# Performance work log

Hardware: AMD Instinct MI355X
Metric: run time of the kernel (lower is better)

The kernel has to match this reference:

```python
import jax, jax.numpy as jnp
import numpy as np

H = 512          # hidden_size
E = 2 * H        # bidirectional embed dim
NH = 8           # attention heads
HD = E // NH     # head dim = 128
SEQ = 10         # hard-coded seq_len in forward
IN = 512         # input_size
OUT = 256        # output_size


def _gru_dir(gi, Whh, bhh, reverse):
    # gi: [B,S,3H] precomputed input-side gate pre-activations
    if reverse:
        gi = gi[:, ::-1]
    B = gi.shape[0]
    h0 = jnp.zeros((B, H), gi.dtype)

    def step(h, gi_t):
        gh = h @ Whh.T + bhh                      # [B,3H]
        ir, iz, inn = jnp.split(gi_t, 3, axis=-1)
        hr, hz, hn = jnp.split(gh, 3, axis=-1)
        r = jax.nn.sigmoid(ir + hr)
        z = jax.nn.sigmoid(iz + hz)
        n = jnp.tanh(inn + r * hn)
        h_new = (1.0 - z) * n + z * h
        return h_new, h_new

    _, hs = jax.lax.scan(step, h0, jnp.swapaxes(gi, 0, 1))
    hs = jnp.swapaxes(hs, 0, 1)                   # [B,S,H]
    if reverse:
        hs = hs[:, ::-1]
    return hs


def _bi_gru_layer(x_seq, Wih, Whh, bih, bhh):
    # Wih: [2, 3H, in]; dir 0 = forward, dir 1 = backward
    outs = []
    for d, rev in ((0, False), (1, True)):
        gi = jnp.einsum('bsi,gi->bsg', x_seq, Wih[d]) + bih[d]
        outs.append(_gru_dir(gi, Whh[d], bhh[d], rev))
    return jnp.concatenate(outs, axis=-1)         # [B,S,2H]


def _attention(x, in_proj_w, in_proj_b, out_proj_w, out_proj_b):
    B, S, _ = x.shape
    qkv = x @ in_proj_w.T + in_proj_b             # [B,S,3E]
    q, k, v = jnp.split(qkv, 3, axis=-1)
    q = q.reshape(B, S, NH, HD)
    k = k.reshape(B, S, NH, HD)
    v = v.reshape(B, S, NH, HD)
    scores = jnp.einsum('bqhd,bkhd->bhqk', q, k) / jnp.sqrt(jnp.asarray(HD, x.dtype))
    attn = jax.nn.softmax(scores, axis=-1)
    o = jnp.einsum('bhqk,bkhd->bqhd', attn, v).reshape(B, S, E)
    return o @ out_proj_w.T + out_proj_b


def _forward(x, Wp, bp, Wih0, Whh0, bih0, bhh0, Wih1, Whh1, bih1, bhh1,
             in_proj_w, in_proj_b, out_proj_w, out_proj_b, W1, b1, W2, b2):
    x_proj = x @ Wp.T + bp                        # [B,H]
    phases = 2.0 * np.pi * np.arange(SEQ) / SEQ
    cos = jnp.asarray(np.cos(phases), x.dtype)    # [S]
    sin = jnp.asarray(np.sin(phases), x.dtype)
    rolled = jnp.roll(x_proj, shift=1, axis=-1)
    x_seq = (x_proj[:, None, :] * (1.0 + 0.1 * cos[None, :, None])
             + 0.05 * sin[None, :, None] * rolled[:, None, :])  # [B,S,H]
    h1 = _bi_gru_layer(x_seq, Wih0, Whh0, bih0, bhh0)           # [B,S,2H]
    gru_out = _bi_gru_layer(h1, Wih1, Whh1, bih1, bhh1)         # [B,S,2H]
    attn_out = _attention(gru_out, in_proj_w, in_proj_b, out_proj_w, out_proj_b)
    aggregated = jnp.mean(gru_out + attn_out, axis=1)           # [B,2H]
    hid = jnp.tanh(aggregated @ W1.T + b1)                      # [B,128]
    return hid @ W2.T + b2                                      # [B,OUT]


def setup_inputs() -> dict:
    key = jax.random.key(0)
    ks = jax.random.split(key, 24)
    s = 1.0 / np.sqrt(H)
    u = lambda k, shape: jax.random.uniform(k, shape, jnp.float32, -s, s)
    return {
        'x': jax.random.normal(ks[0], (4096, IN), jnp.float32),
        'Wp': u(ks[1], (H, IN)), 'bp': u(ks[2], (H,)),
        'Wih0': u(ks[3], (2, 3 * H, H)), 'Whh0': u(ks[4], (2, 3 * H, H)),
        'bih0': u(ks[5], (2, 3 * H)), 'bhh0': u(ks[6], (2, 3 * H)),
        'Wih1': u(ks[7], (2, 3 * H, 2 * H)), 'Whh1': u(ks[8], (2, 3 * H, H)),
        'bih1': u(ks[9], (2, 3 * H)), 'bhh1': u(ks[10], (2, 3 * H)),
        'in_proj_w': u(ks[11], (3 * E, E)), 'in_proj_b': u(ks[12], (3 * E,)),
        'out_proj_w': u(ks[13], (E, E)), 'out_proj_b': u(ks[14], (E,)),
        'W1': u(ks[15], (128, E)), 'b1': u(ks[16], (128,)),
        'W2': u(ks[17], (OUT, 128)), 'b2': u(ks[18], (OUT,)),
    }


def reference(x, Wp, bp, Wih0, Whh0, bih0, bhh0, Wih1, Whh1, bih1, bhh1,
              in_proj_w, in_proj_b, out_proj_w, out_proj_b, W1, b1, W2, b2):
    return _forward(x, Wp, bp, Wih0, Whh0, bih0, bhh0, Wih1, Whh1, bih1, bhh1,
                    in_proj_w, in_proj_b, out_proj_w, out_proj_b, W1, b1, W2, b2)
```

## Files before the change

### kernel.cpp

```cpp
#include <hip/hip_runtime.h>
#include <math.h>


#define SEQ 10

typedef unsigned short bf16u;
typedef __attribute__((ext_vector_type(8))) short short8v;
typedef __attribute__((ext_vector_type(4))) float f32x4;

#define AS1 __attribute__((address_space(1)))
#define AS3 __attribute__((address_space(3)))

__device__ __forceinline__ float b2f(bf16u u) {
    union { unsigned int i; float f; } v; v.i = ((unsigned int)u) << 16; return v.f;
}
__device__ __forceinline__ bf16u f2b(float f) {
    union { float f; unsigned int i; } v; v.f = f;
    unsigned int r = (v.i + 0x7FFFu + ((v.i >> 16) & 1u)) >> 16;
    return (bf16u)r;
}
__device__ __forceinline__ float fast_sigm(float x) { return 1.0f / (1.0f + __expf(-x)); }
__device__ __forceinline__ float fast_tanh(float x) {
    float e = __expf(-2.0f * x);
    return 2.0f / (1.0f + e) - 1.0f;
}

__global__ void cvt_f2b(const float* __restrict__ src, bf16u* __restrict__ dst, int n4)
{
    int i = blockIdx.x * 256 + threadIdx.x;
    if (i < n4) {
        float4 v = ((const float4*)src)[i];
        ushort4 u; u.x = f2b(v.x); u.y = f2b(v.y); u.z = f2b(v.z); u.w = f2b(v.w);
        ((ushort4*)dst)[i] = u;
    }
}

template <typename TC>
__global__ __launch_bounds__(512) void gemm_mfma256(
    const bf16u* __restrict__ A, long long sAz, int lda,
    const bf16u* __restrict__ W, long long sWz,
    const float* __restrict__ bias, long long sBz,
    TC* __restrict__ C, long long sCz, int ldc,
    int K, int act)
{
    __shared__ bf16u As[2][256 * 64];
    __shared__ bf16u Ws[2][256 * 64];

    const int z = blockIdx.z;
    A += (long long)z * sAz;
    W += (long long)z * sWz;
    C += (long long)z * sCz;
    const float* bz = bias ? (bias + (long long)z * sBz) : nullptr;

    const int gx = gridDim.x;
    const int nwg = gx * gridDim.y;
    const int orig = blockIdx.y * gx + blockIdx.x;
    const int q = nwg >> 3, rres = nwg & 7;
    const int xcd = orig & 7, loc = orig >> 3;
    const int wgid = (xcd < rres ? xcd * (q + 1) : rres * (q + 1) + (xcd - rres) * q) + loc;
    const int bm = (wgid / gx) * 256;
    const int bn = (wgid % gx) * 256;

    const int tid = threadIdx.x;
    const int lane = tid & 63;
    const int w = tid >> 6;
    const int wm = w >> 2;
    const int wn = w & 3;
    const int l15 = lane & 15;
    const int lk8 = (lane >> 4) * 8;
    const int swz = (l15 & 7) << 3;

    f32x4 acc[8][4];
#pragma unroll
    for (int i = 0; i < 8; ++i)
#pragma unroll
        for (int j = 0; j < 4; ++j)
#pragma unroll
            for (int r = 0; r < 4; ++r) acc[i][j][r] = 0.0f;

    const int srow = lane >> 3;
    const int scol = ((lane & 7) ^ srow) * 8;
    const bf16u* Ag[4];
    const bf16u* Wg[4];
    int loff[4];
#pragma unroll
    for (int p = 0; p < 4; ++p) {
        const int r = p * 64 + w * 8 + srow;
        Ag[p] = A + (long long)(bm + r) * lda + scol;
        Wg[p] = W + (long long)(bn + r) * K + scol;
        loff[p] = (p * 8 + w) * 512;
    }

    auto stage = [&](int kt, int b) {
        const long long k1 = (long long)kt << 6;
#pragma unroll
        for (int p = 0; p < 4; ++p) {
            __builtin_amdgcn_global_load_lds((const AS1 void*)(Ag[p] + k1),
                (AS3 void*)(&As[b][loff[p]]), 16, 0, 0);
            __builtin_amdgcn_global_load_lds((const AS1 void*)(Wg[p] + k1),
                (AS3 void*)(&Ws[b][loff[p]]), 16, 0, 0);
        }
    };
    auto compute = [&](int b) {
#pragma unroll
        for (int ks = 0; ks < 2; ++ks) {
            const int ko = (ks * 32 + lk8) ^ swz;
            short8v af[8], bfr[4];
#pragma unroll
            for (int i = 0; i < 8; ++i)
                af[i] = *(const short8v*)(&As[b][(wm * 128 + i * 16 + l15) * 64 + ko]);
#pragma unroll
            for (int i = 0; i < 4; ++i)
                bfr[i] = *(const short8v*)(&Ws[b][(wn * 64 + i * 16 + l15) * 64 + ko]);
#pragma unroll
            for (int mi = 0; mi < 8; ++mi)
#pragma unroll
                for (int ni = 0; ni < 4; ++ni)
                    acc[mi][ni] = __builtin_amdgcn_mfma_f32_16x16x32_bf16(
                        af[mi], bfr[ni], acc[mi][ni], 0, 0, 0);
        }
    };

    const int nt = K >> 6;

    stage(0, 0);
    stage(1, 1);

    for (int t = 0; t < nt - 1; ++t) {
        asm volatile("s_waitcnt vmcnt(8)" ::: "memory");
        __builtin_amdgcn_s_barrier();
        asm volatile("" ::: "memory");
        compute(t & 1);
        asm volatile("" ::: "memory");
        __builtin_amdgcn_s_barrier();
        if (t + 2 < nt) stage(t + 2, t & 1);
    }
    asm volatile("s_waitcnt vmcnt(0)" ::: "memory");
    __builtin_amdgcn_s_barrier();
    compute((nt - 1) & 1);

    const int r0 = (lane >> 4) * 4;
#pragma unroll
    for (int mi = 0; mi < 8; ++mi) {
#pragma unroll
        for (int ni = 0; ni < 4; ++ni) {
            const int col = bn + wn * 64 + ni * 16 + l15;
            float badd = bz ? bz[col] : 0.0f;
#pragma unroll
            for (int r = 0; r < 4; ++r) {
                const long long row = bm + wm * 128 + mi * 16 + r0 + r;
                float v = acc[mi][ni][r] + badd;
                if (act) v = tanhf(v);
                if constexpr (sizeof(TC) == 4) ((float*)C)[row * ldc + col] = v;
                else                           ((bf16u*)C)[row * ldc + col] = f2b(v);
            }
        }
    }
}

template <typename TC>
__global__ __launch_bounds__(256) void gemm_mfma128p(
    const bf16u* __restrict__ A, long long sAz, int lda,
    const bf16u* __restrict__ W, long long sWz,
    const float* __restrict__ bias, long long sBz,
    TC* __restrict__ C, long long sCz, int ldc,
    int K, int act)
{
    __shared__ bf16u As[2][128 * 64];
    __shared__ bf16u Ws[2][128 * 64];

    const int z = blockIdx.z;
    A += (long long)z * sAz;
    W += (long long)z * sWz;
    C += (long long)z * sCz;
    const float* bz = bias ? (bias + (long long)z * sBz) : nullptr;

    const int gx = gridDim.x;
    const int nwg = gx * gridDim.y;
    const int orig = blockIdx.y * gx + blockIdx.x;
    const int q = nwg >> 3, rres = nwg & 7;
    const int xcd = orig & 7, loc = orig >> 3;
    const int wgid = (xcd < rres ? xcd * (q + 1) : rres * (q + 1) + (xcd - rres) * q) + loc;
    const int bm = (wgid / gx) * 128;
    const int bn = (wgid % gx) * 128;

    const int tid = threadIdx.x;
    const int lane = tid & 63;
    const int w = tid >> 6;
    const int wm = w >> 1;
    const int wn = w & 1;
    const int l15 = lane & 15;
    const int lk8 = (lane >> 4) * 8;
    const int swz = (l15 & 7) << 3;

    f32x4 acc[4][4];
#pragma unroll
    for (int i = 0; i < 4; ++i)
#pragma unroll
        for (int j = 0; j < 4; ++j)
#pragma unroll
            for (int r = 0; r < 4; ++r) acc[i][j][r] = 0.0f;

    const int srow = lane >> 3;
    const int scol = ((lane & 7) ^ srow) * 8;
    const bf16u* Ag[4];
    const bf16u* Wg[4];
    int loff[4];
#pragma unroll
    for (int p = 0; p < 4; ++p) {
        const int r = p * 32 + w * 8 + srow;
        Ag[p] = A + (long long)(bm + r) * lda + scol;
        Wg[p] = W + (long long)(bn + r) * K + scol;
        loff[p] = (p * 32 + w * 8) * 64;
    }

    auto stage = [&](int kt, int b) {
        const long long k1 = (long long)kt << 6;
#pragma unroll
        for (int p = 0; p < 4; ++p) {
            __builtin_amdgcn_global_load_lds((const AS1 void*)(Ag[p] + k1),
                (AS3 void*)(&As[b][loff[p]]), 16, 0, 0);
            __builtin_amdgcn_global_load_lds((const AS1 void*)(Wg[p] + k1),
                (AS3 void*)(&Ws[b][loff[p]]), 16, 0, 0);
        }
    };
    auto compute = [&](int b) {
#pragma unroll
        for (int ks = 0; ks < 2; ++ks) {
            const int ko = (ks * 32 + lk8) ^ swz;
            short8v af[4], bfr[4];
#pragma unroll
            for (int i = 0; i < 4; ++i)
                af[i] = *(const short8v*)(&As[b][(wm * 64 + i * 16 + l15) * 64 + ko]);
#pragma unroll
            for (int i = 0; i < 4; ++i)
                bfr[i] = *(const short8v*)(&Ws[b][(wn * 64 + i * 16 + l15) * 64 + ko]);
            __builtin_amdgcn_s_setprio(1);
#pragma unroll
            for (int mi = 0; mi < 4; ++mi)
#pragma unroll
                for (int ni = 0; ni < 4; ++ni)
                    acc[mi][ni] = __builtin_amdgcn_mfma_f32_16x16x32_bf16(
                        af[mi], bfr[ni], acc[mi][ni], 0, 0, 0);
            __builtin_amdgcn_s_setprio(0);
        }
    };

    const int nt = K >> 6;

    stage(0, 0);
    stage(1, 1);

    for (int t = 0; t < nt - 1; ++t) {
        asm volatile("s_waitcnt vmcnt(8)" ::: "memory");
        __builtin_amdgcn_s_barrier();
        asm volatile("" ::: "memory");
        compute(t & 1);
        asm volatile("" ::: "memory");
        __builtin_amdgcn_s_barrier();
        if (t + 2 < nt) stage(t + 2, t & 1);
    }
    asm volatile("s_waitcnt vmcnt(0)" ::: "memory");
    __builtin_amdgcn_s_barrier();
    compute((nt - 1) & 1);

    const int r0 = (lane >> 4) * 4;
#pragma unroll
    for (int mi = 0; mi < 4; ++mi) {
#pragma unroll
        for (int ni = 0; ni < 4; ++ni) {
            const int col = bn + wn * 64 + ni * 16 + l15;
            float badd = bz ? bz[col] : 0.0f;
#pragma unroll
            for (int r = 0; r < 4; ++r) {
                const long long row = bm + wm * 64 + mi * 16 + r0 + r;
                float v = acc[mi][ni][r] + badd;
                if (act) v = tanhf(v);
                if constexpr (sizeof(TC) == 4) ((float*)C)[row * ldc + col] = v;
                else                           ((bf16u*)C)[row * ldc + col] = f2b(v);
            }
        }
    }
}

template <typename TC>
__global__ __launch_bounds__(256) void gemm_mfma(
    const bf16u* __restrict__ A, long long sAz, int lda,
    const bf16u* __restrict__ W, long long sWz,
    const float* __restrict__ bias, long long sBz,
    TC* __restrict__ C, long long sCz, int ldc,
    int K, int act)
{
    __shared__ bf16u As[128 * 64];
    __shared__ bf16u Ws[128 * 64];

    const int z = blockIdx.z;
    A += (long long)z * sAz;
    W += (long long)z * sWz;
    C += (long long)z * sCz;
    const float* bz = bias ? (bias + (long long)z * sBz) : nullptr;

    const int gx = gridDim.x;
    const int nwg = gx * gridDim.y;
    const int orig = blockIdx.y * gx + blockIdx.x;
    const int q = nwg >> 3, rres = nwg & 7;
    const int xcd = orig & 7, loc = orig >> 3;
    const int wgid = (xcd < rres ? xcd * (q + 1) : rres * (q + 1) + (xcd - rres) * q) + loc;
    const int bm = (wgid / gx) * 128;
    const int bn = (wgid % gx) * 128;

    const int tid = threadIdx.x;
    const int lane = tid & 63;
    const int wave = tid >> 6;
    const int wr = (wave >> 1) * 64;
    const int wc = (wave & 1) * 64;
    const int l15 = lane & 15;
    const int lk8 = (lane >> 4) * 8;

    f32x4 acc[4][4];
#pragma unroll
    for (int i = 0; i < 4; ++i)
#pragma unroll
        for (int j = 0; j < 4; ++j)
#pragma unroll
            for (int r = 0; r < 4; ++r) acc[i][j][r] = 0.0f;

    const int sr = wave * 32 + (lane >> 3);
    const int sc = (lane & 7) * 8;
    const bf16u* Ag = A + (long long)(bm + sr) * lda + sc;
    const bf16u* Wg = W + (long long)(bn + sr) * K + sc;
    bf16u* Al = As + wave * 32 * 64;
    bf16u* Wl = Ws + wave * 32 * 64;

    for (int k0 = 0; k0 < K; k0 += 64) {
#pragma unroll
        for (int p = 0; p < 4; ++p) {
            __builtin_amdgcn_global_load_lds(
                (const AS1 void*)(Ag + k0 + (long long)(8 * p) * lda),
                (AS3 void*)(Al + 8 * p * 64), 16, 0, 0);
            __builtin_amdgcn_global_load_lds(
                (const AS1 void*)(Wg + k0 + (long long)(8 * p) * K),
                (AS3 void*)(Wl + 8 * p * 64), 16, 0, 0);
        }
        __syncthreads();
#pragma unroll
        for (int ks = 0; ks < 2; ++ks) {
            short8v af[4], bfr[4];
#pragma unroll
            for (int i = 0; i < 4; ++i)
                af[i] = *(const short8v*)(As + (wr + i * 16 + l15) * 64 + ks * 32 + lk8);
#pragma unroll
            for (int i = 0; i < 4; ++i)
                bfr[i] = *(const short8v*)(Ws + (wc + i * 16 + l15) * 64 + ks * 32 + lk8);
#pragma unroll
            for (int mi = 0; mi < 4; ++mi)
#pragma unroll
                for (int ni = 0; ni < 4; ++ni)
                    acc[mi][ni] = __builtin_amdgcn_mfma_f32_16x16x32_bf16(
                        af[mi], bfr[ni], acc[mi][ni], 0, 0, 0);
        }
        __syncthreads();
    }

    const int r0 = (lane >> 4) * 4;
#pragma unroll
    for (int mi = 0; mi < 4; ++mi) {
#pragma unroll
        for (int ni = 0; ni < 4; ++ni) {
            const int col = bn + wc + ni * 16 + l15;
            float badd = bz ? bz[col] : 0.0f;
#pragma unroll
            for (int r = 0; r < 4; ++r) {
                const long long row = bm + wr + mi * 16 + r0 + r;
                float v = acc[mi][ni][r] + badd;
                if (act) v = tanhf(v);
                if constexpr (sizeof(TC) == 4) ((float*)C)[row * ldc + col] = v;
                else                           ((bf16u*)C)[row * ldc + col] = f2b(v);
            }
        }
    }
}

template <int LAYER, bool FIRST>
__global__ __launch_bounds__(256) void gru_step(
    const bf16u* __restrict__ Hb,
    const bf16u* __restrict__ Whh,
    const float* __restrict__ bhh,
    const bf16u* __restrict__ P0,
    const bf16u* __restrict__ P1,
    const float* __restrict__ bih,
    const bf16u* __restrict__ GIT,
    const float* __restrict__ hprev,
    float* __restrict__ hnext,
    bf16u* __restrict__ hnextb,
    bf16u* __restrict__ hout,
    int t, int CB)
{
    __shared__ bf16u As[2][64 * 64];
    __shared__ bf16u Ws[2][96 * 64];

    const int z = blockIdx.z;
    const int bn = blockIdx.x * 32;
    const int bm = blockIdx.y * 64;
    const int tid = threadIdx.x;
    const int lane = tid & 63;
    const int wave = tid >> 6;
    const int wm = wave >> 1;
    const int wn = wave & 1;
    const int l15 = lane & 15;
    const int lk8 = (lane >> 4) * 8;
    const int swz = (l15 & 7) << 3;

    f32x4 acc[3][2];
#pragma unroll
    for (int g = 0; g < 3; ++g)
#pragma unroll
        for (int i = 0; i < 2; ++i)
#pragma unroll
            for (int r = 0; r < 4; ++r) acc[g][i][r] = 0.0f;

    if constexpr (!FIRST) {
        const bf16u* hsrc = Hb + (long long)z * CB * 512;
        const bf16u* wsrc = Whh + (long long)z * 1536 * 512;

        const int srow = lane >> 3;
        const int sc = ((lane & 7) ^ srow) * 8;
        const bf16u* Ag = hsrc + (long long)(bm + 16 * wave + srow) * 512 + sc;
        const bf16u* Wg[3];
#pragma unroll
        for (int p = 0; p < 3; ++p) {
            const int lr = 24 * wave + 8 * p + srow;
            const int g = lr >> 5, c = lr & 31;
            Wg[p] = wsrc + (long long)(g * 512 + bn + c) * 512 + sc;
        }

        auto stage = [&](int kt, int b) {
            const long long k0 = (long long)kt << 6;
#pragma unroll
            for (int p = 0; p < 2; ++p)
                __builtin_amdgcn_global_load_lds(
                    (const AS1 void*)(Ag + k0 + (long long)(8 * p) * 512),
                    (AS3 void*)(&As[b][(16 * wave + 8 * p) * 64]), 16, 0, 0);
#pragma unroll
            for (int p = 0; p < 3; ++p)
                __builtin_amdgcn_global_load_lds(
                    (const AS1 void*)(Wg[p] + k0),
                    (AS3 void*)(&Ws[b][(24 * wave + 8 * p) * 64]), 16, 0, 0);
        };
        auto compute = [&](int b) {
#pragma unroll
            for (int ks = 0; ks < 2; ++ks) {
                const int ko = (ks * 32 + lk8) ^ swz;
                short8v af[2], bf[3];
#pragma unroll
                for (int mi = 0; mi < 2; ++mi)
                    af[mi] = *(const short8v*)(&As[b][(wm * 32 + mi * 16 + l15) * 64 + ko]);
#pragma unroll
                for (int g = 0; g < 3; ++g)
                    bf[g] = *(const short8v*)(&Ws[b][(g * 32 + wn * 16 + l15) * 64 + ko]);
                __builtin_amdgcn_s_setprio(1);
#pragma unroll
                for (int g = 0; g < 3; ++g)
#pragma unroll
                    for (int mi = 0; mi < 2; ++mi)
                        acc[g][mi] = __builtin_amdgcn_mfma_f32_16x16x32_bf16(
                            af[mi], bf[g], acc[g][mi], 0, 0, 0);
                __builtin_amdgcn_s_setprio(0);
            }
        };

        stage(0, 0);
        stage(1, 1);
        for (int kt = 0; kt < 7; ++kt) {
            asm volatile("s_waitcnt vmcnt(5)" ::: "memory");
            __builtin_amdgcn_s_barrier();
            asm volatile("" ::: "memory");
            compute(kt & 1);
            asm volatile("" ::: "memory");
            __builtin_amdgcn_s_barrier();
            if (kt + 2 < 8) stage(kt + 2, kt & 1);
        }
        asm volatile("s_waitcnt vmcnt(0)" ::: "memory");
        __builtin_amdgcn_s_barrier();
        compute(1);
    }

    const int r0 = (lane >> 4) * 4;
    const int s = z ? (SEQ - 1 - t) : t;
    float c0 = 0.0f, c1 = 0.0f;
    if (LAYER == 0) {
        float ph = 0.6283185307179586f * (float)s;
        c0 = 1.0f + 0.1f * cosf(ph);
        c1 = 0.05f * sinf(ph);
    }

    const int j = bn + wn * 16 + l15;
    const float bh0 = bhh[z * 1536 + j];
    const float bh1 = bhh[z * 1536 + 512 + j];
    const float bh2 = bhh[z * 1536 + 1024 + j];
    float bi0 = 0, bi1 = 0, bi2 = 0;
    if (LAYER == 0) {
        bi0 = bih[z * 1536 + j];
        bi1 = bih[z * 1536 + 512 + j];
        bi2 = bih[z * 1536 + 1024 + j];
    }

#pragma unroll
    for (int mi = 0; mi < 2; ++mi) {
#pragma unroll
        for (int rr = 0; rr < 4; ++rr) {
            const int m = bm + wm * 32 + mi * 16 + r0 + rr;
            float gr = acc[0][mi][rr] + bh0;
            float gz = acc[1][mi][rr] + bh1;
            float gn = acc[2][mi][rr] + bh2;
            float ir, iz, inn;
            if (LAYER == 0) {
                const bf16u* p0 = P0 + (long long)m * 3072 + z * 1536 + j;
                const bf16u* p1 = P1 + (long long)m * 3072 + z * 1536 + j;
                ir  = c0 * b2f(p0[0])    + c1 * b2f(p1[0])    + bi0;
                iz  = c0 * b2f(p0[512])  + c1 * b2f(p1[512])  + bi1;
                inn = c0 * b2f(p0[1024]) + c1 * b2f(p1[1024]) + bi2;
            } else {
                const bf16u* gi = GIT + (((long long)z * CB + m) * SEQ + s) * 1536 + j;
                ir = b2f(gi[0]); iz = b2f(gi[512]); inn = b2f(gi[1024]);
            }
            const long long ho = ((long long)z * CB + m) * 512 + j;
            float r  = fast_sigm(ir + gr);
            float zz = fast_sigm(iz + gz);
            float n  = fast_tanh(inn + r * gn);
            float hnew;
            if constexpr (FIRST) hnew = (1.0f - zz) * n;
            else                 hnew = (1.0f - zz) * n + zz * hprev[ho];
            hnext[ho]  = hnew;
            hnextb[ho] = f2b(hnew);
            hout[((long long)m * SEQ + s) * 1024 + z * 512 + j] = f2b(hnew);
        }
    }
}

__global__ void roll_b(const bf16u* __restrict__ xp, bf16u* __restrict__ rl)
{
    int idx = blockIdx.x * 256 + threadIdx.x;
    int i = idx & 511;
    int b = idx >> 9;
    rl[(size_t)b * 512 + i] = xp[(size_t)b * 512 + ((i + 511) & 511)];
}

__global__ __launch_bounds__(128) void attn_kernel(const bf16u* __restrict__ qkv,
                                                   bf16u* __restrict__ osum)
{
    const int bh = blockIdx.x;
    const int h = bh & 7;
    const int bl = bh >> 3;
    const int tid = threadIdx.x;

    __shared__ float Q[SEQ][128], Kx[SEQ][128], V[SEQ][128], Amat[SEQ][SEQ];

    const bf16u* base = qkv + (size_t)bl * SEQ * 3072 + h * 128;
#pragma unroll
    for (int s = 0; s < SEQ; ++s) {
        Q[s][tid]  = b2f(base[s * 3072 + tid]);
        Kx[s][tid] = b2f(base[s * 3072 + 1024 + tid]);
        V[s][tid]  = b2f(base[s * 3072 + 2048 + tid]);
    }
    __syncthreads();

    if (tid < SEQ * SEQ) {
        int q = tid / SEQ, k = tid % SEQ;
        float acc = 0.0f;
#pragma unroll 8
        for (int d0 = 0; d0 < 128; ++d0) acc += Q[q][d0] * Kx[k][d0];
        Amat[q][k] = acc * 0.08838834764831845f;
    }
    __syncthreads();

    if (tid < SEQ) {
        float m = -1e30f;
#pragma unroll
        for (int k = 0; k < SEQ; ++k) m = fmaxf(m, Amat[tid][k]);
        float e[SEQ], ssum = 0.0f;
#pragma unroll
        for (int k = 0; k < SEQ; ++k) { e[k] = expf(Amat[tid][k] - m); ssum += e[k]; }
        float inv = 1.0f / ssum;
#pragma unroll
        for (int k = 0; k < SEQ; ++k) Amat[tid][k] = e[k] * inv;
    }
    __syncthreads();

    float os = 0.0f;
#pragma unroll
    for (int q = 0; q < SEQ; ++q) {
        float acc = 0.0f;
#pragma unroll
        for (int k = 0; k < SEQ; ++k) acc += Amat[q][k] * V[k][tid];
        os += acc;
    }
    osum[(size_t)bl * 1024 + h * 128 + tid] = f2b(0.1f * os);
}

__global__ void gmean_kernel(const bf16u* __restrict__ go, const float* __restrict__ att,
                             bf16u* __restrict__ agg)
{
    int idx = blockIdx.x * 256 + threadIdx.x;
    int j4 = (idx & 255) * 4;
    int bl = idx >> 8;
    const bf16u* g = go + (size_t)bl * (SEQ * 1024) + j4;
    float4 a = *(const float4*)(att + (size_t)bl * 1024 + j4);
    float s0 = 0, s1 = 0, s2 = 0, s3 = 0;
#pragma unroll
    for (int t = 0; t < SEQ; ++t) {
        ushort4 gv = *(const ushort4*)(g + t * 1024);
        s0 += b2f(gv.x); s1 += b2f(gv.y); s2 += b2f(gv.z); s3 += b2f(gv.w);
    }
    ushort4 u;
    u.x = f2b(0.1f * s0 + a.x); u.y = f2b(0.1f * s1 + a.y);
    u.z = f2b(0.1f * s2 + a.z); u.w = f2b(0.1f * s3 + a.w);
    *(ushort4*)(agg + (size_t)bl * 1024 + j4) = u;
}

extern "C" void kernel_launch(void* const* d_in, const int* in_sizes, int n_in,
                              void* d_out, int out_size, void* d_ws, size_t ws_size,
                              hipStream_t stream)
{
    const float* x    = (const float*)d_in[0];
    const float* Wp   = (const float*)d_in[1];
    const float* bp   = (const float*)d_in[2];
    const float* Wih0 = (const float*)d_in[3];
    const float* Whh0 = (const float*)d_in[4];
    const float* bih0 = (const float*)d_in[5];
    const float* bhh0 = (const float*)d_in[6];
    const float* Wih1 = (const float*)d_in[7];
    const float* Whh1 = (const float*)d_in[8];
    const float* bih1 = (const float*)d_in[9];
    const float* bhh1 = (const float*)d_in[10];
    const float* ipw  = (const float*)d_in[11];
    const float* ipb  = (const float*)d_in[12];
    const float* opw  = (const float*)d_in[13];
    const float* opb  = (const float*)d_in[14];
    const float* W1   = (const float*)d_in[15];
    const float* b1   = (const float*)d_in[16];
    const float* W2   = (const float*)d_in[17];
    const float* b2   = (const float*)d_in[18];
    float* out = (float*)d_out;

    const long long WOVER = 9437184LL;
    const long long WALL  = 24969216LL;
    int CB = 0;
    for (int c = 4096; c >= 128; c >>= 1)
        if (WOVER + (long long)c * 114688 <= (long long)ws_size) { CB = c; break; }
    if (CB == 0) return;
    const bool resident = (WALL + (long long)CB * 114688 <= (long long)ws_size);
    const long long WB = resident ? WALL : WOVER;

    bf16u* wreg = (bf16u*)d_ws;
    bf16u *Wpb, *Wih0b, *Whh0b, *Wih1b, *Whh1b, *ipwb, *opwb, *W1b, *W2b;
    if (resident) {
        Wpb   = wreg;
        Wih0b = wreg + 262144;
        Whh0b = wreg + 1835008;
        Wih1b = wreg + 3407872;
        Whh1b = wreg + 6553600;
        ipwb  = wreg + 8126464;
        opwb  = wreg + 11272192;
        W1b   = wreg + 12320768;
        W2b   = wreg + 12451840;
    } else {
        Wpb   = wreg;
        Wih0b = wreg + 262144;
        Whh0b = wreg + 1835008;
        Wih1b = wreg;
        Whh1b = wreg + 3145728;
        ipwb  = wreg;
        opwb  = wreg + 3145728;
        W1b   = wreg + 4194304;
        W2b   = wreg + 4325376;
    }

    char* A0 = (char*)d_ws + WB;
    bf16u* H1c = (bf16u*)A0;
    bf16u* GOc = (bf16u*)(A0 + 20480LL * CB);
    char*  U   = A0 + 40960LL * CB;
    bf16u* P0    = (bf16u*)U;
    bf16u* P1    = (bf16u*)(U + 6144LL * CB);
    bf16u* XB    = (bf16u*)(U + 12288LL * CB);
    bf16u* XPb   = (bf16u*)(U + 13312LL * CB);
    bf16u* RLb   = (bf16u*)(U + 14336LL * CB);
    bf16u* GIT   = (bf16u*)U;
    char*  HC    = U + 61440LL * CB;
    bf16u* QKV   = (bf16u*)U;
    bf16u* OSUMb = (bf16u*)(U + 61440LL * CB);
    float* ATT   = (float*)A0;
    bf16u* AGGb  = (bf16u*)(A0 + 10240LL * CB);
    bf16u* HIDb  = (bf16u*)(A0 + 12288LL * CB);

    const dim3 blk(256);
    const int MB = CB / 128;

    auto cvt = [&](const float* s, bf16u* d, long long nfloats) {
        int n4 = (int)(nfloats / 4);
        cvt_f2b<<<(n4 + 255) / 256, blk, 0, stream>>>(s, d, n4);
    };

    if (resident) {
        cvt(Wp,   Wpb,   512LL * 512);
        cvt(Wih0, Wih0b, 2LL * 1536 * 512);
        cvt(Whh0, Whh0b, 2LL * 1536 * 512);
        cvt(Wih1, Wih1b, 2LL * 1536 * 1024);
        cvt(Whh1, Whh1b, 2LL * 1536 * 512);
        cvt(ipw,  ipwb,  3072LL * 1024);
        cvt(opw,  opwb,  1024LL * 1024);
        cvt(W1,   W1b,   128LL * 1024);
        cvt(W2,   W2b,   256LL * 128);
    }

    for (int c0 = 0; c0 < 4096; c0 += CB) {
        cvt(x + (long long)c0 * 512, XB, (long long)CB * 512);
        if (!resident) {
            cvt(Wp,   Wpb,   512LL * 512);
            cvt(Wih0, Wih0b, 2LL * 1536 * 512);
            cvt(Whh0, Whh0b, 2LL * 1536 * 512);
        }

        gemm_mfma<bf16u><<<dim3(4, MB, 1), blk, 0, stream>>>(
            XB, 0, 512, Wpb, 0, bp, 0, XPb, 0, 512, 512, 0);
        roll_b<<<CB * 2, blk, 0, stream>>>(XPb, RLb);
        gemm_mfma128p<bf16u><<<dim3(24, MB, 2), blk, 0, stream>>>(
            XPb, (long long)CB * 512, 512, Wih0b, 0, nullptr, 0,
            P0, (long long)CB * 3072, 3072, 512, 0);

        for (int t = 0; t < SEQ; ++t) {
            const int rb = t & 1;
            float* hprev  = (float*)(HC + (long long)rb * 6144 * CB);
            bf16u* Hbr    = (bf16u*)(HC + (long long)rb * 6144 * CB + 4096LL * CB);
            float* hnext  = (float*)(HC + (long long)(1 - rb) * 6144 * CB);
            bf16u* hnextb = (bf16u*)(HC + (long long)(1 - rb) * 6144 * CB + 4096LL * CB);
            if (t == 0)
                gru_step<0, true><<<dim3(16, CB / 64, 2), blk, 0, stream>>>(
                    Hbr, Whh0b, bhh0, P0, P1, bih0, nullptr,
                    hprev, hnext, hnextb, H1c, t, CB);
            else
                gru_step<0, false><<<dim3(16, CB / 64, 2), blk, 0, stream>>>(
                    Hbr, Whh0b, bhh0, P0, P1, bih0, nullptr,
                    hprev, hnext, hnextb, H1c, t, CB);
        }

        if (!resident) {
            cvt(Wih1, Wih1b, 2LL * 1536 * 1024);
            cvt(Whh1, Whh1b, 2LL * 1536 * 512);
        }
        gemm_mfma256<bf16u><<<dim3(6, CB * 10 / 256, 2), dim3(512), 0, stream>>>(
            H1c, 0, 1024, Wih1b, 1536LL * 1024, bih1, 1536,
            GIT, (long long)CB * SEQ * 1536, 1536, 1024, 0);

        for (int t = 0; t < SEQ; ++t) {
            const int rb = t & 1;
            float* hprev  = (float*)(HC + (long long)rb * 6144 * CB);
            bf16u* Hbr    = (bf16u*)(HC + (long long)rb * 6144 * CB + 4096LL * CB);
            float* hnext  = (float*)(HC + (long long)(1 - rb) * 6144 * CB);
            bf16u* hnextb = (bf16u*)(HC + (long long)(1 - rb) * 6144 * CB + 4096LL * CB);
            if (t == 0)
                gru_step<1, true><<<dim3(16, CB / 64, 2), blk, 0, stream>>>(
                    Hbr, Whh1b, bhh1, nullptr, nullptr, nullptr, GIT,
                    hprev, hnext, hnextb, GOc, t, CB);
            else
                gru_step<1, false><<<dim3(16, CB / 64, 2), blk, 0, stream>>>(
                    Hbr, Whh1b, bhh1, nullptr, nullptr, nullptr, GIT,
                    hprev, hnext, hnextb, GOc, t, CB);
        }

        if (!resident) {
            cvt(ipw, ipwb, 3072LL * 1024);
            cvt(opw, opwb, 1024LL * 1024);
            cvt(W1,  W1b,  128LL * 1024);
            cvt(W2,  W2b,  256LL * 128);
        }
        gemm_mfma256<bf16u><<<dim3(12, CB * 10 / 256, 1), dim3(512), 0, stream>>>(
            GOc, 0, 1024, ipwb, 0, ipb, 0, QKV, 0, 3072, 1024, 0);
        attn_kernel<<<CB * 8, dim3(128), 0, stream>>>(QKV, OSUMb);
        gemm_mfma128p<float><<<dim3(8, MB, 1), blk, 0, stream>>>(
            OSUMb, 0, 1024, opwb, 0, opb, 0, ATT, 0, 1024, 1024, 0);
        gmean_kernel<<<CB, blk, 0, stream>>>(GOc, ATT, AGGb);
        gemm_mfma<bf16u><<<dim3(1, MB, 1), blk, 0, stream>>>(
            AGGb, 0, 1024, W1b, 0, b1, 0, HIDb, 0, 128, 1024, 1);
        gemm_mfma<float><<<dim3(2, MB, 1), blk, 0, stream>>>(
            HIDb, 0, 128, W2b, 0, b2, 0, out + (long long)c0 * 256, 0, 256, 128, 0);
    }
}
```

Before: 2.056 ms.

## Restructure GEMM mainloop into 4-stage K=32 pipeline with interleaved loads and setprio

The 256x256 bf16 GEMM kernel changes from a double-buffered K=64 tile to a four-slot ring of K=32 tiles with a three-deep prefetch. Each step splits into two half-tile MFMA phases, and the global-to-LDS loads for a future tile are issued between those phases. MFMA sections are wrapped in s_setprio so matrix work is favoured over other waves' memory issue. The XOR swizzle is redone for the 32-wide rows. The aim is to hide memory latency and LDS waits better, at the cost of more barriers per K step and hand-tuned vmcnt counts that must stay exact.

New measurement: 2.108 ms. 2.5% more time.

```diff
diff --git a/kernel.cpp b/kernel.cpp
--- a/kernel.cpp
+++ b/kernel.cpp
@@ -43,8 +43,8 @@
     TC* __restrict__ C, long long sCz, int ldc,
     int K, int act)
 {
-    __shared__ bf16u As[2][256 * 64];
-    __shared__ bf16u Ws[2][256 * 64];
+    __shared__ bf16u As4[4][256 * 32];
+    __shared__ bf16u Ws4[4][256 * 32];
 
     const int z = blockIdx.z;
     A += (long long)z * sAz;
@@ -67,8 +67,7 @@
     const int wm = w >> 2;
     const int wn = w & 3;
     const int l15 = lane & 15;
-    const int lk8 = (lane >> 4) * 8;
-    const int swz = (l15 & 7) << 3;
+    const int sl8 = (((lane >> 4) ^ ((l15 >> 1) & 3)) << 3);
 
     f32x4 acc[8][4];
 #pragma unroll
@@ -78,66 +77,90 @@
 #pragma unroll
             for (int r = 0; r < 4; ++r) acc[i][j][r] = 0.0f;
 
-    const int srow = lane >> 3;
-    const int scol = ((lane & 7) ^ srow) * 8;
-    const bf16u* Ag[4];
-    const bf16u* Wg[4];
-    int loff[4];
-#pragma unroll
-    for (int p = 0; p < 4; ++p) {
-        const int r = p * 64 + w * 8 + srow;
-        Ag[p] = A + (long long)(bm + r) * lda + scol;
-        Wg[p] = W + (long long)(bn + r) * K + scol;
-        loff[p] = (p * 8 + w) * 512;
-    }
-
-    auto stage = [&](int kt, int b) {
-        const long long k1 = (long long)kt << 6;
-#pragma unroll
-        for (int p = 0; p < 4; ++p) {
-            __builtin_amdgcn_global_load_lds((const AS1 void*)(Ag[p] + k1),
-                (AS3 void*)(&As[b][loff[p]]), 16, 0, 0);
-            __builtin_amdgcn_global_load_lds((const AS1 void*)(Wg[p] + k1),
-                (AS3 void*)(&Ws[b][loff[p]]), 16, 0, 0);
-        }
+    const int srow2 = lane >> 2;
+    const int scol2 = (((lane & 3) ^ ((lane >> 3) & 3)) << 3);
+    const bf16u* Ag[2];
+    const bf16u* Wg[2];
+    int la[2];
+#pragma unroll
+    for (int l = 0; l < 2; ++l) {
+        Ag[l] = A + (long long)(bm + l * 128 + w * 16 + srow2) * lda + scol2;
+        Wg[l] = W + (long long)(bn + l * 128 + w * 16 + srow2) * (long long)K + scol2;
+        la[l] = (l * 128 + w * 16) * 32;
+    }
+
+    const int NG = K >> 5;
+
+    auto issue = [&](int h, int l) {
+        const int s = h & 3;
+        __builtin_amdgcn_global_load_lds((const AS1 void*)(Ag[l] + (long long)h * 32),
+            (AS3 void*)(&As4[s][la[l]]), 16, 0, 0);
+        __builtin_amdgcn_global_load_lds((const AS1 void*)(Wg[l] + (long long)h * 32),
+            (AS3 void*)(&Ws4[s][la[l]]), 16, 0, 0);
     };
-    auto compute = [&](int b) {
-#pragma unroll
-        for (int ks = 0; ks < 2; ++ks) {
-            const int ko = (ks * 32 + lk8) ^ swz;
-            short8v af[8], bfr[4];
-#pragma unroll
-            for (int i = 0; i < 8; ++i)
-                af[i] = *(const short8v*)(&As[b][(wm * 128 + i * 16 + l15) * 64 + ko]);
-#pragma unroll
-            for (int i = 0; i < 4; ++i)
-                bfr[i] = *(const short8v*)(&Ws[b][(wn * 64 + i * 16 + l15) * 64 + ko]);
-#pragma unroll
-            for (int mi = 0; mi < 8; ++mi)
-#pragma unroll
-                for (int ni = 0; ni < 4; ++ni)
-                    acc[mi][ni] = __builtin_amdgcn_mfma_f32_16x16x32_bf16(
-                        af[mi], bfr[ni], acc[mi][ni], 0, 0, 0);
-        }
-    };
-
-    const int nt = K >> 6;
-
-    stage(0, 0);
-    stage(1, 1);
-
-    for (int t = 0; t < nt - 1; ++t) {
-        asm volatile("s_waitcnt vmcnt(8)" ::: "memory");
+
+#pragma unroll
+    for (int h = 0; h < 3; ++h) { issue(h, 0); issue(h, 1); }
+    asm volatile("s_waitcnt vmcnt(8)" ::: "memory");
+    __builtin_amdgcn_s_barrier();
+    asm volatile("" ::: "memory");
+
+    short8v bfr[4];
+
+    for (int g = 0; g < NG; ++g) {
+        const bf16u* Ab = &As4[g & 3][0];
+        const bf16u* Wb = &Ws4[g & 3][0];
+        const bool pf = (g + 3 < NG);
+
+        short8v af0[4];
+#pragma unroll
+        for (int i = 0; i < 4; ++i)
+            af0[i] = *(const short8v*)(Ab + (wm * 128 + i * 16 + l15) * 32 + sl8);
+#pragma unroll
+        for (int i = 0; i < 4; ++i)
+            bfr[i] = *(const short8v*)(Wb + (wn * 64 + i * 16 + l15) * 32 + sl8);
+        if (pf) issue(g + 3, 0);
+        asm volatile("" ::: "memory");
         __builtin_amdgcn_s_barrier();
         asm volatile("" ::: "memory");
-        compute(t & 1);
+        __builtin_amdgcn_s_setprio(1);
+#pragma unroll
+        for (int mi = 0; mi < 4; ++mi)
+#pragma unroll
+            for (int ni = 0; ni < 4; ++ni)
+                acc[mi][ni] = __builtin_amdgcn_mfma_f32_16x16x32_bf16(
+                    af0[mi], bfr[ni], acc[mi][ni], 0, 0, 0);
+        __builtin_amdgcn_s_setprio(0);
         asm volatile("" ::: "memory");
         __builtin_amdgcn_s_barrier();
-        if (t + 2 < nt) stage(t + 2, t & 1);
-    }
-    asm volatile("s_waitcnt vmcnt(0)" ::: "memory");
-    __builtin_amdgcn_s_barrier();
-    compute((nt - 1) & 1);
+        asm volatile("" ::: "memory");
+
+        short8v af1[4];
+#pragma unroll
+        for (int i = 0; i < 4; ++i)
+            af1[i] = *(const short8v*)(Ab + (wm * 128 + (i + 4) * 16 + l15) * 32 + sl8);
+        if (pf) issue(g + 3, 1);
+        asm volatile("" ::: "memory");
+        __builtin_amdgcn_s_barrier();
+        asm volatile("" ::: "memory");
+        __builtin_amdgcn_s_setprio(1);
+#pragma unroll
+        for (int mi = 0; mi < 4; ++mi)
+#pragma unroll
+            for (int ni = 0; ni < 4; ++ni)
+                acc[mi + 4][ni] = __builtin_amdgcn_mfma_f32_16x16x32_bf16(
+                    af1[mi], bfr[ni], acc[mi + 4][ni], 0, 0, 0);
+        __builtin_amdgcn_s_setprio(0);
+
+        if (g + 1 < NG) {
+            if (g + 3 < NG)      asm volatile("s_waitcnt vmcnt(8)" ::: "memory");
+            else if (g + 2 < NG) asm volatile("s_waitcnt vmcnt(4)" ::: "memory");
+            else                 asm volatile("s_waitcnt vmcnt(0)" ::: "memory");
+            asm volatile("" ::: "memory");
+            __builtin_amdgcn_s_barrier();
+            asm volatile("" ::: "memory");
+        }
+    }
 
     const int r0 = (lane >> 4) * 4;
 #pragma unroll
```
